# Performance work log

Measured on AMD Instinct MI355X. Metric: run time of the kernel, lower is better.

The kernel has to match this reference:

```python
import jax, jax.numpy as jnp
import numpy as np

B_, HEADS, G, DH = 16, 8, 64, 64
N = 101 * 31              # mesh points H*W
DM = HEADS * DH           # 512 = Hydra d_model = d_inner (expand=1)
HEADDIM = 64
NH = DM // HEADDIM        # 8 SSM heads inside Hydra
DSTATE, DCONV = 1, 3
DINPROJ = 2 * DM + 2 * DSTATE + 2 * NH   # 1042
CONVDIM = DM + 2 * DSTATE                # 514
DIM = 512                 # module output dim


def setup_inputs():
    key = jax.random.key(0)
    ks = jax.random.split(key, 12)
    s = lambda k, shape, sc=0.02: jax.random.normal(k, shape, jnp.float32) * sc
    return dict(
        slice_token=jax.random.normal(ks[0], (B_, HEADS, G, DH), jnp.float32),
        slice_weights=jax.random.uniform(ks[1], (B_, HEADS, N, G), jnp.float32),
        w_in=s(ks[2], (DINPROJ, DM)),
        conv_w=s(ks[3], (CONVDIM, DCONV), 0.1),
        conv_b=s(ks[4], (CONVDIM,), 0.1),
        dt_bias=s(ks[5], (NH,), 0.5),
        A_log=jnp.log(jnp.linspace(1.0, 8.0, NH)).astype(jnp.float32),
        D=jnp.ones((NH,), jnp.float32),
        fc_D_w=s(ks[6], (NH, DM)),
        norm_w=jnp.ones((DM,), jnp.float32),
        w_out=s(ks[7], (DM, DM)),
        to_out_w=s(ks[8], (DIM, DM)),
        to_out_b=jnp.zeros((DIM,), jnp.float32),
    )


def _silu(x):
    return x * jax.nn.sigmoid(x)


def _hydra(u, w_in, conv_w, conv_b, dt_bias, A_log, D, fc_D_w, norm_w, w_out):
    # Bidirectional Mamba-2 style quasiseparable mixer (Hydra), d_state=1, ngroups=1
    b, L, _ = u.shape
    zxbcdt = u @ w_in.T                                   # (b,L,1042)
    z = zxbcdt[..., :DM]
    xBC = zxbcdt[..., DM:DM + CONVDIM]
    dt = zxbcdt[..., DM + CONVDIM:]                       # (b,L,2*NH)
    # fw dt + time-flipped bw dt, stacked on batch
    dt = jnp.concatenate([dt[..., :NH], dt[..., NH:][:, ::-1]], axis=0)  # (2b,L,NH)
    dt = jax.nn.softplus(dt + dt_bias)
    # causal depthwise conv (kernel 3, left pad d_conv-1) + SiLU
    xp = jnp.pad(xBC, ((0, 0), (DCONV - 1, 0), (0, 0)))
    xBC = conv_b + sum(conv_w[:, k] * xp[:, k:k + L] for k in range(DCONV))
    xBC = _silu(xBC)
    x = xBC[..., :DM]
    Bv = xBC[..., DM:DM + DSTATE]                         # (b,L,1)
    Cv = xBC[..., DM + DSTATE:]                           # (b,L,1)
    x_og = x
    x2 = jnp.concatenate([x, x[:, ::-1]], axis=0)         # (2b,L,DM)
    B2 = jnp.concatenate([Bv, Bv[:, ::-1]], axis=0)
    C2 = jnp.concatenate([Cv, Cv[:, ::-1]], axis=0)
    xh = x2.reshape(2 * b, L, NH, HEADDIM)
    A = -jnp.exp(A_log)                                   # (NH,)
    a = jnp.exp(dt * A)[..., None]                        # (2b,L,NH,1)
    bterm = dt[..., None] * B2[..., None, :] * xh         # (2b,L,NH,HEADDIM)
    aB = jnp.broadcast_to(a, bterm.shape)

    def comb(c1, c2):
        a1, b1 = c1
        a2, b2 = c2
        return a1 * a2, a2 * b1 + b2

    _, hst = jax.lax.associative_scan(comb, (aB, bterm), axis=1)
    y = (hst * C2[..., None, :]).reshape(2 * b, L, DM)
    # strict shift (off-diagonal quasiseparable parts)
    y = jnp.roll(y, 1, axis=1).at[:, 0, :].set(0.0)
    y_fw, y_bw = y[:b], y[b:, ::-1]
    # input-dependent diagonal term
    dcoef = x_og @ fc_D_w.T + D                           # (b,L,NH)
    dterm = (x_og.reshape(b, L, NH, HEADDIM) * dcoef[..., None]).reshape(b, L, DM)
    y = y_fw + y_bw + dterm
    # gated RMSNorm (norm after gate)
    y = y * _silu(z)
    y = y * jax.lax.rsqrt(jnp.mean(y * y, axis=-1, keepdims=True) + 1e-5) * norm_w
    return y @ w_out.T


def reference(slice_token, slice_weights, w_in, conv_w, conv_b, dt_bias, A_log, D,
              fc_D_w, norm_w, w_out, to_out_w, to_out_b):
    b, h, g, c = slice_token.shape
    inp = slice_token
    u = slice_token.transpose(0, 2, 1, 3).reshape(b, g, h * c)          # b g (h c)
    out = _hydra(u, w_in, conv_w, conv_b, dt_bias, A_log, D, fc_D_w, norm_w, w_out)
    outp = out.reshape(b, g, h, c).transpose(0, 2, 1, 3)                # b h g c
    out_x = jnp.einsum('bhgc,bhng->bhnc', outp, slice_weights)
    out_x = out_x.transpose(0, 2, 1, 3).reshape(b, out_x.shape[2], h * c)
    return out_x @ to_out_w.T + to_out_b, inp, outp
```

## Files before the change

kernel.cpp:

```cpp
#include <hip/hip_runtime.h>
#include <math.h>

#define B_ 16
#define HEADS_ 8
#define G_ 64
#define DH_ 64
#define N_ 3131
#define DM_ 512
#define NH_ 8
#define DINPROJ_ 1042
#define CONVDIM_ 514
#define DIM_ 512

#define OUT0_OFS 0
#define OUT1_OFS (B_*N_*DIM_)
#define OUT2_OFS (B_*N_*DIM_ + B_*HEADS_*G_*DH_)

#define SW_ELEMS (B_*HEADS_*N_*64)

typedef __attribute__((ext_vector_type(8))) short short8;
typedef __attribute__((ext_vector_type(4))) float f32x4;

__device__ __forceinline__ float siluf(float v){ return v / (1.f + expf(-v)); }
__device__ __forceinline__ float softplusf(float v){ return (v > 20.f) ? v : log1pf(expf(v)); }
__device__ __forceinline__ unsigned short f2bf(float f){
    unsigned int u = __float_as_uint(f);
    unsigned int r = (u + 0x7fffu + ((u >> 16) & 1u)) >> 16;
    return (unsigned short)r;
}

__global__ void k0_cvt(const float* __restrict__ sw, unsigned short* __restrict__ swb) {
    int i = blockIdx.x * 256 + threadIdx.x;
    const float4* p = (const float4*)(sw + (size_t)i * 8);
    float4 v0 = p[0], v1 = p[1];
    short8 o;
    o[0]=f2bf(v0.x); o[1]=f2bf(v0.y); o[2]=f2bf(v0.z); o[3]=f2bf(v0.w);
    o[4]=f2bf(v1.x); o[5]=f2bf(v1.y); o[6]=f2bf(v1.z); o[7]=f2bf(v1.w);
    *(short8*)(swb + (size_t)i * 8) = o;
}

__global__ void k1_inproj(const float* __restrict__ st,
                          const float* __restrict__ w_in,
                          float* __restrict__ zx) {
    __shared__ float Ast[64][68];
    __shared__ float Bs[64][68];
    int j0 = blockIdx.x * 64;
    int b  = blockIdx.y;
    int tid = threadIdx.x, tx = tid & 15, ty = tid >> 4;
    float acc[4][4];
#pragma unroll
    for (int i = 0; i < 4; i++)
#pragma unroll
        for (int j = 0; j < 4; j++) acc[i][j] = 0.f;

    for (int h = 0; h < 8; h++) {
        const float* Ab = st + ((size_t)(b*8 + h) * 64) * 64;
        for (int i = tid; i < 1024; i += 256) {
            int l = i >> 4, cq = i & 15;
            float4 v = *(const float4*)(Ab + l*64 + cq*4);
            Ast[cq*4+0][l] = v.x; Ast[cq*4+1][l] = v.y;
            Ast[cq*4+2][l] = v.z; Ast[cq*4+3][l] = v.w;
        }
        for (int i = tid; i < 1024; i += 256) {
            int jl = i >> 4, cq = i & 15;
            int j = j0 + jl;
            float4 v = make_float4(0.f,0.f,0.f,0.f);
            if (j < DINPROJ_) v = *(const float4*)(w_in + (size_t)j*DM_ + h*64 + cq*4);
            Bs[cq*4+0][jl] = v.x; Bs[cq*4+1][jl] = v.y;
            Bs[cq*4+2][jl] = v.z; Bs[cq*4+3][jl] = v.w;
        }
        __syncthreads();
#pragma unroll 8
        for (int k = 0; k < 64; k++) {
            float4 av = *(const float4*)&Ast[k][ty*4];
            float4 bv = *(const float4*)&Bs[k][tx*4];
            float aa[4] = {av.x, av.y, av.z, av.w};
            float bb[4] = {bv.x, bv.y, bv.z, bv.w};
#pragma unroll
            for (int i = 0; i < 4; i++)
#pragma unroll
                for (int j = 0; j < 4; j++) acc[i][j] += aa[i]*bb[j];
        }
        __syncthreads();
    }
#pragma unroll
    for (int i = 0; i < 4; i++) {
        int bl = b*64 + ty*4 + i;
#pragma unroll
        for (int j = 0; j < 4; j++) {
            int jj = j0 + tx*4 + j;
            if (jj < DINPROJ_) zx[(size_t)bl*DINPROJ_ + jj] = acc[i][j];
        }
    }
}

__global__ void k2_conv(const float* __restrict__ zx,
                        const float* __restrict__ conv_w,
                        const float* __restrict__ conv_b,
                        const float* __restrict__ dt_bias,
                        const float* __restrict__ A_log,
                        const float* __restrict__ fc_D_w,
                        const float* __restrict__ Dvec,
                        float* __restrict__ x, float* __restrict__ zs,
                        float* __restrict__ Cv, float* __restrict__ tblf,
                        float* __restrict__ dco) {
    int bl = blockIdx.x; int b = bl >> 6, l = bl & 63;
    __shared__ float sx[DM_];
    __shared__ float sBv;
    const float* zrow = zx + (size_t)bl * DINPROJ_;

    for (int ch = threadIdx.x; ch < CONVDIM_; ch += 256) {
        float v = conv_b[ch];
#pragma unroll
        for (int k = 0; k < 3; k++) {
            int t = l - 2 + k;
            if (t >= 0) v += conv_w[ch*3 + k] * zx[(size_t)(b*G_ + t) * DINPROJ_ + DM_ + ch];
        }
        float sv = siluf(v);
        if (ch < DM_)      { x[(size_t)bl*DM_ + ch] = sv; sx[ch] = sv; }
        else if (ch == DM_){ sBv = sv; }
        else               { Cv[bl] = sv; }
    }
    for (int d = threadIdx.x; d < DM_; d += 256) {
        zs[(size_t)bl*DM_ + d] = siluf(zrow[d]);
    }
    __syncthreads();
    if (threadIdx.x < 16) {
        int i = threadIdx.x; int h = i & 7;
        float dt = softplusf(zrow[DM_ + CONVDIM_ + i] + dt_bias[h]);
        float Ah = -expf(A_log[h]);
        float a  = expf(dt * Ah);
        float bb = dt * sBv;
        float* t4 = tblf + ((size_t)bl*NH_ + h)*4;
        if (i < 8) { t4[0] = a; t4[1] = bb; }
        else       { t4[2] = a; t4[3] = bb; }
    }
    {
        int h = threadIdx.x >> 5, l32 = threadIdx.x & 31;
        const float* fr = fc_D_w + (size_t)h * DM_;
        float s = 0.f;
#pragma unroll
        for (int q = 0; q < 4; q++) {
            int d = q*128 + l32*4;
            float4 w4 = *(const float4*)(fr + d);
            float4 x4 = *(const float4*)(&sx[d]);
            s += w4.x*x4.x + w4.y*x4.y + w4.z*x4.z + w4.w*x4.w;
        }
#pragma unroll
        for (int o = 16; o > 0; o >>= 1) s += __shfl_down(s, o, 32);
        if (l32 == 0) dco[bl*NH_ + h] = s + Dvec[h];
    }
}

__global__ void k3_scan(const float* __restrict__ x, const float* __restrict__ Cv,
                        const float* __restrict__ tblf, const float* __restrict__ dco,
                        float* __restrict__ yfw, float* __restrict__ ybw) {
    int bh = blockIdx.x; int b = bh >> 3, h = bh & 7;
    int dir = blockIdx.y;
    int c = threadIdx.x;
    __shared__ float sA[64], sB[64], sC[64], sD[64];
    {
        int bl = b*64 + c;
        const float* t4 = tblf + ((size_t)bl*NH_ + h)*4;
        sA[c] = dir ? t4[2] : t4[0];
        sB[c] = dir ? t4[3] : t4[1];
        sC[c] = Cv[bl];
        sD[c] = dco[bl*NH_ + h];
    }
    __syncthreads();
    const float* xr = x + (size_t)(b*64)*DM_ + h*64 + c;
    if (dir == 0) {
        float* yw = yfw + (size_t)(b*64)*DM_ + h*64 + c;
        float state = 0.f;
        float xv = xr[0];
#pragma unroll 4
        for (int t = 0; t < 64; t++) {
            float xn = (t < 63) ? xr[(t+1)*DM_] : 0.f;
            float val = xv * sD[t];
            if (t > 0) val += state * sC[t-1];
            yw[t*DM_] = val;
            state = sA[t]*state + sB[t]*xv;
            xv = xn;
        }
    } else {
        float* yw = ybw + (size_t)(b*64)*DM_ + h*64 + c;
        float state = 0.f;
        float xv = xr[63*DM_];
#pragma unroll 4
        for (int s = 63; s >= 0; s--) {
            float xn = (s > 0) ? xr[(s-1)*DM_] : 0.f;
            float val = (s < 63) ? state * sC[s+1] : 0.f;
            yw[s*DM_] = val;
            state = sA[s]*state + sB[s]*xv;
            xv = xn;
        }
    }
}

__global__ void k4a_rms(const float* __restrict__ yfw, const float* __restrict__ ybw,
                        const float* __restrict__ zs, const float* __restrict__ norm_w,
                        float* __restrict__ yn) {
    int bl = blockIdx.x;
    __shared__ float red[4];
    float vv[2]; float ss = 0.f;
#pragma unroll
    for (int r = 0; r < 2; r++) {
        size_t i = (size_t)bl*DM_ + threadIdx.x + r*256;
        float v = (yfw[i] + ybw[i]) * zs[i];
        vv[r] = v; ss += v*v;
    }
#pragma unroll
    for (int o = 32; o > 0; o >>= 1) ss += __shfl_down(ss, o, 64);
    if ((threadIdx.x & 63) == 0) red[threadIdx.x >> 6] = ss;
    __syncthreads();
    float scale = rsqrtf((red[0]+red[1]+red[2]+red[3]) / (float)DM_ + 1e-5f);
#pragma unroll
    for (int r = 0; r < 2; r++) {
        int d = threadIdx.x + r*256;
        yn[(size_t)bl*DM_ + d] = vv[r] * scale * norm_w[d];
    }
}

__global__ void k4b_wout(const float* __restrict__ yn,
                         const float* __restrict__ w_out,
                         float* __restrict__ om, float* __restrict__ out2) {
    __shared__ float Ast[64][68];
    __shared__ float Bs[64][68];
    int j0 = blockIdx.x * 64;
    int b  = blockIdx.y;
    int tid = threadIdx.x, tx = tid & 15, ty = tid >> 4;
    float acc[4][4];
#pragma unroll
    for (int i = 0; i < 4; i++)
#pragma unroll
        for (int j = 0; j < 4; j++) acc[i][j] = 0.f;

    for (int kt = 0; kt < 8; kt++) {
        const float* Ab = yn + (size_t)(b*64)*DM_ + kt*64;
        for (int i = tid; i < 1024; i += 256) {
            int l = i >> 4, cq = i & 15;
            float4 v = *(const float4*)(Ab + (size_t)l*DM_ + cq*4);
            Ast[cq*4+0][l] = v.x; Ast[cq*4+1][l] = v.y;
            Ast[cq*4+2][l] = v.z; Ast[cq*4+3][l] = v.w;
        }
        for (int i = tid; i < 1024; i += 256) {
            int jl = i >> 4, cq = i & 15;
            float4 v = *(const float4*)(w_out + (size_t)(j0 + jl)*DM_ + kt*64 + cq*4);
            Bs[cq*4+0][jl] = v.x; Bs[cq*4+1][jl] = v.y;
            Bs[cq*4+2][jl] = v.z; Bs[cq*4+3][jl] = v.w;
        }
        __syncthreads();
#pragma unroll 8
        for (int k = 0; k < 64; k++) {
            float4 av = *(const float4*)&Ast[k][ty*4];
            float4 bv = *(const float4*)&Bs[k][tx*4];
            float aa[4] = {av.x, av.y, av.z, av.w};
            float bb[4] = {bv.x, bv.y, bv.z, bv.w};
#pragma unroll
            for (int i = 0; i < 4; i++)
#pragma unroll
                for (int j = 0; j < 4; j++) acc[i][j] += aa[i]*bb[j];
        }
        __syncthreads();
    }
#pragma unroll
    for (int i = 0; i < 4; i++) {
        int l = ty*4 + i, bl = b*64 + l;
        float4 v = make_float4(acc[i][0], acc[i][1], acc[i][2], acc[i][3]);
        *(float4*)(om + (size_t)bl*DM_ + j0 + tx*4) = v;
        *(float4*)(out2 + (((size_t)(b*8 + blockIdx.x)*64 + l) << 6) + tx*4) = v;
    }
}

__global__ void k5_P(const float* __restrict__ om,
                     const float* __restrict__ to_out_w,
                     unsigned short* __restrict__ Pbf) {
    __shared__ float Ast[64][68];
    __shared__ float Bs[64][68];
    int d0 = blockIdx.x * 64;
    int h  = blockIdx.y;
    int b  = blockIdx.z;
    int tid = threadIdx.x, tx = tid & 15, ty = tid >> 4;

    for (int i = tid; i < 1024; i += 256) {
        int dl = i >> 4, cq = i & 15;
        float4 v = *(const float4*)(to_out_w + (size_t)(d0 + dl)*DM_ + h*64 + cq*4);
        Ast[cq*4+0][dl] = v.x; Ast[cq*4+1][dl] = v.y;
        Ast[cq*4+2][dl] = v.z; Ast[cq*4+3][dl] = v.w;
    }
    for (int i = tid; i < 1024; i += 256) {
        int gl = i >> 4, cq = i & 15;
        float4 v = *(const float4*)(om + (size_t)(b*G_ + gl)*DM_ + h*64 + cq*4);
        Bs[cq*4+0][gl] = v.x; Bs[cq*4+1][gl] = v.y;
        Bs[cq*4+2][gl] = v.z; Bs[cq*4+3][gl] = v.w;
    }
    __syncthreads();

    float acc[4][4];
#pragma unroll
    for (int i = 0; i < 4; i++)
#pragma unroll
        for (int j = 0; j < 4; j++) acc[i][j] = 0.f;
#pragma unroll 8
    for (int k = 0; k < 64; k++) {
        float4 av = *(const float4*)&Ast[k][ty*4];
        float4 bv = *(const float4*)&Bs[k][tx*4];
        float aa[4] = {av.x, av.y, av.z, av.w};
        float bb[4] = {bv.x, bv.y, bv.z, bv.w};
#pragma unroll
        for (int i = 0; i < 4; i++)
#pragma unroll
            for (int j = 0; j < 4; j++) acc[i][j] += aa[i]*bb[j];
    }

#pragma unroll
    for (int i = 0; i < 4; i++) {
        int d = d0 + ty*4 + i;
        ushort4 o;
        o.x = f2bf(acc[i][0]); o.y = f2bf(acc[i][1]);
        o.z = f2bf(acc[i][2]); o.w = f2bf(acc[i][3]);
        *(ushort4*)(Pbf + ((size_t)(b*512) + d)*512 + h*64 + tx*4) = o;
    }
}

__global__ __launch_bounds__(256) void k6_bf(
        const unsigned short* __restrict__ swb,
        const unsigned short* __restrict__ Pbf,
        const float* __restrict__ bias,
        float* __restrict__ out0) {
    __shared__ unsigned short As[128*64];
    __shared__ unsigned short Bs[128*64];
    int wg  = blockIdx.x;
    int fid = (wg & 7)*200 + (wg >> 3);
    int dt  = fid & 3;
    int t2  = fid >> 2;
    int nt  = t2 % 25;
    int b   = t2 / 25;
    int d0 = dt * 128;
    int n0 = nt * 128;
    int tid = threadIdx.x;
    int lane = tid & 63, wid = tid >> 6;
    int wm = wid & 1, wn = wid >> 1;
    int quad = lane >> 4, m16 = lane & 15;
    int lrow = lane >> 3;
    int lsw  = ((lane & 7) ^ (lrow & 7)) * 8;

    f32x4 acc[4][4] = {};

    for (int kt = 0; kt < 8; kt++) {
        const unsigned short* Ab = swb + ((size_t)(b*8 + kt) * N_ + n0) * 64;
#pragma unroll
        for (int c = wid; c < 16; c += 4) {
            const unsigned short* ga = Ab + (size_t)(c*8 + lrow)*64 + lsw;
            __builtin_amdgcn_global_load_lds(
                (const __attribute__((address_space(1))) unsigned int*)ga,
                (__attribute__((address_space(3))) unsigned int*)&As[c*512],
                16, 0, 0);
        }
        const unsigned short* Bb = Pbf + ((size_t)(b*512) + d0)*512 + kt*64;
#pragma unroll
        for (int c = wid; c < 16; c += 4) {
            const unsigned short* gp = Bb + (size_t)(c*8 + lrow)*512 + lsw;
            __builtin_amdgcn_global_load_lds(
                (const __attribute__((address_space(1))) unsigned int*)gp,
                (__attribute__((address_space(3))) unsigned int*)&Bs[c*512],
                16, 0, 0);
        }
        __syncthreads();
#pragma unroll
        for (int ks = 0; ks < 2; ks++) {
            int csw = ((ks*4 + quad) ^ (m16 & 7)) * 8;
            short8 av[4], bv[4];
#pragma unroll
            for (int mt = 0; mt < 4; mt++)
                av[mt] = *(short8*)&As[(wm*64 + mt*16 + m16)*64 + csw];
#pragma unroll
            for (int nt2 = 0; nt2 < 4; nt2++)
                bv[nt2] = *(short8*)&Bs[(wn*64 + nt2*16 + m16)*64 + csw];
#pragma unroll
            for (int mt = 0; mt < 4; mt++)
#pragma unroll
                for (int nt2 = 0; nt2 < 4; nt2++)
                    acc[mt][nt2] = __builtin_amdgcn_mfma_f32_16x16x32_bf16(
                        av[mt], bv[nt2], acc[mt][nt2], 0, 0, 0);
        }
        __syncthreads();
    }
#pragma unroll
    for (int nt2 = 0; nt2 < 4; nt2++) {
        int dcol = d0 + wn*64 + nt2*16 + m16;
        float bval = bias[dcol];
#pragma unroll
        for (int mt = 0; mt < 4; mt++) {
#pragma unroll
            for (int r = 0; r < 4; r++) {
                int n = n0 + wm*64 + mt*16 + quad*4 + r;
                if (n < N_)
                    out0[((size_t)b*N_ + n)*DIM_ + dcol] = acc[mt][nt2][r] + bval;
            }
        }
    }
}

__global__ __launch_bounds__(256) void k6_fp(
        const float* __restrict__ sw,
        const unsigned short* __restrict__ Pbf,
        const float* __restrict__ bias,
        float* __restrict__ out0) {
    __shared__ unsigned short As[128*64];
    __shared__ unsigned short Bs[128*64];
    int wg  = blockIdx.x;
    int fid = (wg & 7)*200 + (wg >> 3);
    int dt  = fid & 3;
    int t2  = fid >> 2;
    int nt  = t2 % 25;
    int b   = t2 / 25;
    int d0 = dt * 128;
    int n0 = nt * 128;
    int tid = threadIdx.x;
    int lane = tid & 63, wid = tid >> 6;
    int wm = wid & 1, wn = wid >> 1;
    int quad = lane >> 4, m16 = lane & 15;
    int lrow = lane >> 3;
    int lsw  = ((lane & 7) ^ (lrow & 7)) * 8;

    f32x4 acc[4][4] = {};

    for (int kt = 0; kt < 8; kt++) {
        const float* Ab = sw + ((size_t)(b*8 + kt) * N_ + n0) * 64;
#pragma unroll
        for (int r = 0; r < 8; r++) {
            int f = r*256 + tid;
            int nl = f >> 4;
            float4 v = make_float4(0.f,0.f,0.f,0.f);
            if (n0 + nl < N_) v = ((const float4*)Ab)[f];
            ushort4 o;
            o.x = f2bf(v.x); o.y = f2bf(v.y); o.z = f2bf(v.z); o.w = f2bf(v.w);
            int row = f >> 4, ch = (f & 15) >> 1, hf = f & 1;
            *(ushort4*)&As[row*64 + ((ch ^ (row & 7))*8 + hf*4)] = o;
        }
        const unsigned short* Bb = Pbf + ((size_t)(b*512) + d0)*512 + kt*64;
#pragma unroll
        for (int c = wid; c < 16; c += 4) {
            const unsigned short* gp = Bb + (size_t)(c*8 + lrow)*512 + lsw;
            __builtin_amdgcn_global_load_lds(
                (const __attribute__((address_space(1))) unsigned int*)gp,
                (__attribute__((address_space(3))) unsigned int*)&Bs[c*512],
                16, 0, 0);
        }
        __syncthreads();
#pragma unroll
        for (int ks = 0; ks < 2; ks++) {
            int csw = ((ks*4 + quad) ^ (m16 & 7)) * 8;
            short8 av[4], bv[4];
#pragma unroll
            for (int mt = 0; mt < 4; mt++)
                av[mt] = *(short8*)&As[(wm*64 + mt*16 + m16)*64 + csw];
#pragma unroll
            for (int nt2 = 0; nt2 < 4; nt2++)
                bv[nt2] = *(short8*)&Bs[(wn*64 + nt2*16 + m16)*64 + csw];
#pragma unroll
            for (int mt = 0; mt < 4; mt++)
#pragma unroll
                for (int nt2 = 0; nt2 < 4; nt2++)
                    acc[mt][nt2] = __builtin_amdgcn_mfma_f32_16x16x32_bf16(
                        av[mt], bv[nt2], acc[mt][nt2], 0, 0, 0);
        }
        __syncthreads();
    }
#pragma unroll
    for (int nt2 = 0; nt2 < 4; nt2++) {
        int dcol = d0 + wn*64 + nt2*16 + m16;
        float bval = bias[dcol];
#pragma unroll
        for (int mt = 0; mt < 4; mt++) {
#pragma unroll
            for (int r = 0; r < 4; r++) {
                int n = n0 + wm*64 + mt*16 + quad*4 + r;
                if (n < N_)
                    out0[((size_t)b*N_ + n)*DIM_ + dcol] = acc[mt][nt2][r] + bval;
            }
        }
    }
}

extern "C" void kernel_launch(void* const* d_in, const int* in_sizes, int n_in,
                              void* d_out, int out_size, void* d_ws, size_t ws_size,
                              hipStream_t stream) {
    const float* st      = (const float*)d_in[0];
    const float* sw      = (const float*)d_in[1];
    const float* w_in    = (const float*)d_in[2];
    const float* conv_w  = (const float*)d_in[3];
    const float* conv_b  = (const float*)d_in[4];
    const float* dt_bias = (const float*)d_in[5];
    const float* A_log   = (const float*)d_in[6];
    const float* Dvec    = (const float*)d_in[7];
    const float* fc_D_w  = (const float*)d_in[8];
    const float* norm_w  = (const float*)d_in[9];
    const float* w_out   = (const float*)d_in[10];
    const float* to_out_w= (const float*)d_in[11];
    const float* to_out_b= (const float*)d_in[12];
    float* out = (float*)d_out;
    float* ws  = (float*)d_ws;

    unsigned short* Pbf = (unsigned short*)ws;
    float* base = ws + 2097152;
    float* zx   = base;
    float* xb   = zx  + (size_t)B_*G_*DINPROJ_;
    float* zs   = xb  + (size_t)B_*G_*DM_;
    float* tblf = zs  + (size_t)B_*G_*DM_;
    float* Cv   = tblf+ (size_t)B_*G_*NH_*4;
    float* dco  = Cv  + B_*G_;
    float* yfw  = dco + B_*G_*NH_;
    float* ybw  = yfw + (size_t)B_*G_*DM_;
    float* yn   = ybw + (size_t)B_*G_*DM_;
    float* om   = yn  + (size_t)B_*G_*DM_;
    unsigned short* swb = (unsigned short*)base;
    size_t need_async = (2097152 + (size_t)SW_ELEMS/2 + 64) * sizeof(float);
    bool async_ok = ws_size >= need_async;

    dim3 g1(17, 16);
    k1_inproj<<<g1, 256, 0, stream>>>(st, w_in, zx);
    k2_conv  <<<B_*G_, 256, 0, stream>>>(zx, conv_w, conv_b, dt_bias, A_log,
                                         fc_D_w, Dvec, xb, zs, Cv, tblf, dco);
    dim3 g3(B_*HEADS_, 2);
    k3_scan  <<<g3, 64, 0, stream>>>(xb, Cv, tblf, dco, yfw, ybw);
    k4a_rms  <<<B_*G_, 256, 0, stream>>>(yfw, ybw, zs, norm_w, yn);
    dim3 g4(8, 16);
    k4b_wout <<<g4, 256, 0, stream>>>(yn, w_out, om, out + OUT2_OFS);
    dim3 g5(8, 8, 16);
    k5_P     <<<g5, 256, 0, stream>>>(om, to_out_w, Pbf);
    if (async_ok) {
        k0_cvt<<<SW_ELEMS/8/256, 256, 0, stream>>>(sw, swb);
        k6_bf <<<1600, 256, 0, stream>>>(swb, Pbf, to_out_b, out + OUT0_OFS);
    } else {
        k6_fp <<<1600, 256, 0, stream>>>(sw, Pbf, to_out_b, out + OUT0_OFS);
    }
    hipMemcpyAsync(out + OUT1_OFS, st, (size_t)B_*HEADS_*G_*DH_*sizeof(float),
                   hipMemcpyDeviceToDevice, stream);
}
```

Baseline: 413.8 us.

## Double-buffer k6_bf LDS tiles with half-width K steps and clamped rows

The bf16 output GEMM now splits each 64-wide K tile into two 32-wide halves and double-buffers the A and B tiles in LDS. Async global-to-LDS loads for the next step are issued before the MFMA work on the current step, so each iteration needs one barrier instead of two. Rows past N are clamped to the last valid row rather than read out of bounds, and the swizzle is changed to suit 32-element rows. The workspace size check is enlarged slightly. In exchange the kernel runs twice as many, smaller iterations, with more barriers in total and fewer MFMAs between them.

```diff
diff --git a/kernel.cpp b/kernel.cpp
--- a/kernel.cpp
+++ b/kernel.cpp
@@ -328,8 +328,8 @@
         const unsigned short* __restrict__ Pbf,
         const float* __restrict__ bias,
         float* __restrict__ out0) {
-    __shared__ unsigned short As[128*64];
-    __shared__ unsigned short Bs[128*64];
+    __shared__ unsigned short As[2][128*32];
+    __shared__ unsigned short Bs[2][128*32];
     int wg  = blockIdx.x;
     int fid = (wg & 7)*200 + (wg >> 3);
     int dt  = fid & 3;
@@ -342,49 +342,51 @@
     int lane = tid & 63, wid = tid >> 6;
     int wm = wid & 1, wn = wid >> 1;
     int quad = lane >> 4, m16 = lane & 15;
-    int lrow = lane >> 3;
-    int lsw  = ((lane & 7) ^ (lrow & 7)) * 8;
+    int arow = lane >> 2;
+    int ach  = (((lane & 3) ^ ((arow ^ (arow >> 2)) & 3))) * 8;
+    int csw  = ((quad ^ ((m16 ^ (m16 >> 2)) & 3))) * 8;
 
     f32x4 acc[4][4] = {};
 
-    for (int kt = 0; kt < 8; kt++) {
-        const unsigned short* Ab = swb + ((size_t)(b*8 + kt) * N_ + n0) * 64;
-#pragma unroll
-        for (int c = wid; c < 16; c += 4) {
-            const unsigned short* ga = Ab + (size_t)(c*8 + lrow)*64 + lsw;
+    auto stage = [&](int kt, int nb) {
+        int h = kt >> 1, half = kt & 1;
+        const unsigned short* Abase = swb + ((size_t)(b*8 + h) * N_) * 64 + half*32;
+        const unsigned short* Bbase = Pbf + ((size_t)(b*512) + d0)*512 + kt*32;
+#pragma unroll
+        for (int c = wid; c < 8; c += 4) {
+            int rr = c*16 + arow;
+            int rn = n0 + rr; if (rn > N_-1) rn = N_-1;
             __builtin_amdgcn_global_load_lds(
-                (const __attribute__((address_space(1))) unsigned int*)ga,
-                (__attribute__((address_space(3))) unsigned int*)&As[c*512],
+                (const __attribute__((address_space(1))) unsigned int*)(Abase + (size_t)rn*64 + ach),
+                (__attribute__((address_space(3))) unsigned int*)&As[nb][c*512],
                 16, 0, 0);
-        }
-        const unsigned short* Bb = Pbf + ((size_t)(b*512) + d0)*512 + kt*64;
-#pragma unroll
-        for (int c = wid; c < 16; c += 4) {
-            const unsigned short* gp = Bb + (size_t)(c*8 + lrow)*512 + lsw;
             __builtin_amdgcn_global_load_lds(
-                (const __attribute__((address_space(1))) unsigned int*)gp,
-                (__attribute__((address_space(3))) unsigned int*)&Bs[c*512],
+                (const __attribute__((address_space(1))) unsigned int*)(Bbase + (size_t)rr*512 + ach),
+                (__attribute__((address_space(3))) unsigned int*)&Bs[nb][c*512],
                 16, 0, 0);
         }
-        __syncthreads();
-#pragma unroll
-        for (int ks = 0; ks < 2; ks++) {
-            int csw = ((ks*4 + quad) ^ (m16 & 7)) * 8;
-            short8 av[4], bv[4];
-#pragma unroll
-            for (int mt = 0; mt < 4; mt++)
-                av[mt] = *(short8*)&As[(wm*64 + mt*16 + m16)*64 + csw];
+    };
+
+    stage(0, 0);
+    __syncthreads();
+    int cur = 0;
+    for (int kt = 0; kt < 16; kt++) {
+        if (kt < 15) stage(kt + 1, cur ^ 1);
+        short8 av[4], bv[4];
+#pragma unroll
+        for (int mt = 0; mt < 4; mt++)
+            av[mt] = *(short8*)&As[cur][(wm*64 + mt*16 + m16)*32 + csw];
+#pragma unroll
+        for (int nt2 = 0; nt2 < 4; nt2++)
+            bv[nt2] = *(short8*)&Bs[cur][(wn*64 + nt2*16 + m16)*32 + csw];
+#pragma unroll
+        for (int mt = 0; mt < 4; mt++)
 #pragma unroll
             for (int nt2 = 0; nt2 < 4; nt2++)
-                bv[nt2] = *(short8*)&Bs[(wn*64 + nt2*16 + m16)*64 + csw];
-#pragma unroll
-            for (int mt = 0; mt < 4; mt++)
-#pragma unroll
-                for (int nt2 = 0; nt2 < 4; nt2++)
-                    acc[mt][nt2] = __builtin_amdgcn_mfma_f32_16x16x32_bf16(
-                        av[mt], bv[nt2], acc[mt][nt2], 0, 0, 0);
-        }
-        __syncthreads();
+                acc[mt][nt2] = __builtin_amdgcn_mfma_f32_16x16x32_bf16(
+                    av[mt], bv[nt2], acc[mt][nt2], 0, 0, 0);
+        __syncthreads();
+        cur ^= 1;
     }
 #pragma unroll
     for (int nt2 = 0; nt2 < 4; nt2++) {
@@ -516,7 +518,7 @@
     float* yn   = ybw + (size_t)B_*G_*DM_;
     float* om   = yn  + (size_t)B_*G_*DM_;
     unsigned short* swb = (unsigned short*)base;
-    size_t need_async = (2097152 + (size_t)SW_ELEMS/2 + 64) * sizeof(float);
+    size_t need_async = (2097152 + (size_t)SW_ELEMS/2 + 4096) * sizeof(float);
     bool async_ok = ws_size >= need_async;
 
     dim3 g1(17, 16);
```

Result: no change. 421.4 us (+1.8%).
